# Kernel optimization log

Hardware: AMD Instinct MI355X
Metric: run time of the kernel (lower is better)

Reference implementation:

```python
import jax, jax.numpy as jnp
import numpy as np

N = 50000      # nodes of type 'conn'
E = 250000     # edges per edge type
NT = 3         # number of edge types
H = 3          # num_heads for hidden layers
D1, D2, DO = 64, 64, 32
IN0 = 34       # 8 + 3 + 6 + 17


def setup_inputs() -> dict:
    key = jax.random.key(0)
    ks = jax.random.split(key, 40)
    it = iter(range(40))

    def nrm(shape, scale=0.1):
        return jax.random.normal(ks[next(it)], shape, dtype=jnp.float32) * scale

    inp = {}
    inp["cat_inputs"] = jax.random.randint(ks[next(it)], (N, 3), 0, 5, dtype=jnp.int32)
    inp["cont_inputs"] = jax.random.normal(ks[next(it)], (N, 17), dtype=jnp.float32)
    inp["src"] = jax.random.randint(ks[next(it)], (NT, E), 0, N)
    inp["dst"] = jax.random.randint(ks[next(it)], (NT, E), 0, N)
    # embedding tables
    inp["emb0"] = nrm((14, 8))
    inp["emb1"] = nrm((5, 3))
    inp["emb2"] = nrm((10, 6))
    # layer 1: GATConv(34 -> 64, heads=3) per etype
    inp["W1"] = nrm((NT, IN0, H * D1))
    inp["al1"] = nrm((NT, H, D1))
    inp["ar1"] = nrm((NT, H, D1))
    inp["b1"] = nrm((NT, H * D1))
    # layer 2: GATConv(192 -> 64, heads=3) per etype
    inp["W2"] = nrm((NT, H * D1, H * D2))
    inp["al2"] = nrm((NT, H, D2))
    inp["ar2"] = nrm((NT, H, D2))
    inp["b2"] = nrm((NT, H * D2))
    # output layer: GATConv(192 -> 32, heads=1) per etype
    inp["W3"] = nrm((NT, H * D2, DO))
    inp["al3"] = nrm((NT, 1, DO))
    inp["ar3"] = nrm((NT, 1, DO))
    inp["b3"] = nrm((NT, DO))
    return inp


def _gat(x, W, al, ar, b, src_t, dst_t, heads, out):
    """DGL GATConv: linear -> per-edge LeakyReLU(0.2) attention -> edge softmax
    over incoming edges -> weighted scatter-sum -> +bias -> leaky_relu(0.01)."""
    n = x.shape[0]
    feat = (x @ W).reshape(n, heads, out)          # (N,H,D)
    el = jnp.sum(feat * al, axis=-1)               # (N,H)
    er = jnp.sum(feat * ar, axis=-1)               # (N,H)
    e = jax.nn.leaky_relu(el[src_t] + er[dst_t], 0.2)  # (E,H)
    emax = jax.ops.segment_max(e, dst_t, num_segments=n)   # (N,H), -inf for empty ok
    ee = jnp.exp(e - emax[dst_t])
    den = jax.ops.segment_sum(ee, dst_t, num_segments=n)
    alpha = ee / den[dst_t]                        # (E,H)
    msg = feat[src_t] * alpha[:, :, None]          # (E,H,D)
    rst = jax.ops.segment_sum(msg, dst_t, num_segments=n) + b.reshape(1, heads, out)
    return jax.nn.leaky_relu(rst, 0.01)            # GATConv activation=F.leaky_relu


def reference(cont_inputs, emb0, emb1, emb2,
              W1, al1, ar1, b1, W2, al2, ar2, b2, W3, al3, ar3, b3,
              cat_inputs, src, dst):
    x = jnp.concatenate([emb0[cat_inputs[:, 0]],
                         emb1[cat_inputs[:, 1]],
                         emb2[cat_inputs[:, 2]],
                         cont_inputs], axis=1)     # (N,34)

    def hetero(h, W, al, ar, b, heads, out):
        # HeteroGraphConv(aggregate='mean') over NT edge types, then flatten(1)
        outs = [_gat(h, W[t], al[t], ar[t], b[t], src[t], dst[t], heads, out)
                for t in range(NT)]
        agg = jnp.mean(jnp.stack(outs, 0), axis=0)  # (N,heads,out)
        return agg.reshape(h.shape[0], heads * out)

    h = hetero(x, W1, al1, ar1, b1, H, D1)
    h = hetero(h, W2, al2, ar2, b2, H, D2)
    h = hetero(h, W3, al3, ar3, b3, 1, DO)
    return h
```

## Files before the change

kernel.cpp:

```cpp
#include <hip/hip_runtime.h>

#define NNODES 50000
#define NEDGES 250000
#define NTYPES 3
#define SCAN_B ((NNODES + 255) / 256)
#define LSTR 40

typedef __attribute__((ext_vector_type(8))) short bf16x8;
typedef __attribute__((ext_vector_type(4))) float f32x4;

__device__ __forceinline__ float lrelu(float x, float s) { return x >= 0.f ? x : s * x; }

__device__ __forceinline__ unsigned short bf16_rne(float f) {
    unsigned u = __float_as_uint(f);
    unsigned r = (u + 0x7fffu + ((u >> 16) & 1u)) >> 16;
    return (unsigned short)r;
}
__device__ __forceinline__ float bf16_to_f(unsigned short h) {
    return __uint_as_float((unsigned)h << 16);
}

__global__ void build_x_kernel(const int* __restrict__ cat, const float* __restrict__ cont,
                               const float* __restrict__ e0, const float* __restrict__ e1,
                               const float* __restrict__ e2, short* __restrict__ Ahi,
                               short* __restrict__ Alo) {
    int n = blockIdx.x * 4 + (threadIdx.x >> 6);
    int k = threadIdx.x & 63;
    if (n >= NNODES) return;
    float v = 0.f;
    if (k < 8) v = e0[cat[n * 3 + 0] * 8 + k];
    else if (k < 11) v = e1[cat[n * 3 + 1] * 3 + (k - 8)];
    else if (k < 17) v = e2[cat[n * 3 + 2] * 6 + (k - 11)];
    else if (k < 34) v = cont[n * 17 + (k - 17)];
    unsigned short h = bf16_rne(v);
    float fh = bf16_to_f(h);
    unsigned short l = bf16_rne(v - fh);
    Ahi[(size_t)n * 64 + k] = (short)h;
    Alo[(size_t)n * 64 + k] = (short)l;
}

__global__ void hist_kernel(const int* __restrict__ dst, int* __restrict__ deg) {
    int idx = blockIdx.x * blockDim.x + threadIdx.x;
    if (idx >= NTYPES * NEDGES) return;
    int t = idx / NEDGES;
    atomicAdd(&deg[t * NNODES + dst[idx]], 1);
}

__global__ void scan1_kernel(const int* __restrict__ deg, int* __restrict__ rowptr,
                             int* __restrict__ bsum) {
    __shared__ int sd[256];
    int t = blockIdx.y, b = blockIdx.x, tid = threadIdx.x;
    int n = b * 256 + tid;
    int v = (n < NNODES) ? deg[t * NNODES + n] : 0;
    sd[tid] = v;
    __syncthreads();
    for (int off = 1; off < 256; off <<= 1) {
        int x = 0;
        if (tid >= off) x = sd[tid - off];
        __syncthreads();
        if (tid >= off) sd[tid] += x;
        __syncthreads();
    }
    int incl = sd[tid];
    if (n < NNODES) rowptr[(size_t)t * (NNODES + 1) + n] = incl - v;
    if (tid == 255) bsum[t * SCAN_B + b] = incl;
}

__global__ void scan2_kernel(int* __restrict__ bsum, int* __restrict__ rowptr) {
    int t = threadIdx.x;
    if (t >= NTYPES) return;
    int run = 0;
    for (int i = 0; i < SCAN_B; i++) {
        int v = bsum[t * SCAN_B + i];
        bsum[t * SCAN_B + i] = run;
        run += v;
    }
    rowptr[(size_t)t * (NNODES + 1) + NNODES] = run;
}

__global__ void scan3_kernel(const int* __restrict__ bsum, int* __restrict__ rowptr) {
    int t = blockIdx.y, b = blockIdx.x;
    int n = b * 256 + threadIdx.x;
    if (n < NNODES) rowptr[(size_t)t * (NNODES + 1) + n] += bsum[t * SCAN_B + b];
}

__global__ void scatter_kernel(const int* __restrict__ src, const int* __restrict__ dst,
                               const int* __restrict__ rowptr, int* __restrict__ cursor,
                               int* __restrict__ csrc) {
    int idx = blockIdx.x * blockDim.x + threadIdx.x;
    if (idx >= NTYPES * NEDGES) return;
    int t = idx / NEDGES;
    int s = src[idx], d = dst[idx];
    int pos = rowptr[(size_t)t * (NNODES + 1) + d] + atomicAdd(&cursor[t * NNODES + d], 1);
    csrc[(size_t)t * NEDGES + pos] = s;
}

__global__ void convert_B_kernel(const float* __restrict__ W, short* __restrict__ Bhi,
                                 short* __restrict__ Blo, int Kin, int Kout, int HD, int Mfeat) {
    int idx = blockIdx.x * blockDim.x + threadIdx.x;
    if (idx >= Mfeat * Kout) return;
    int m = idx / Kout, k = idx % Kout;
    int t = m / HD, j = m % HD;
    float a = (k < Kin) ? W[((size_t)t * Kin + k) * HD + j] : 0.f;
    unsigned short h = bf16_rne(a);
    float fh = bf16_to_f(h);
    unsigned short l = bf16_rne(a - fh);
    Bhi[(size_t)m * Kout + k] = (short)h;
    Blo[(size_t)m * Kout + k] = (short)l;
}

__global__ void convert_Bel_kernel(const float* __restrict__ W, const float* __restrict__ alw,
                                   const float* __restrict__ arw, short* __restrict__ Bhi,
                                   short* __restrict__ Blo, int Kin, int Kout, int H, int D,
                                   int Mfeat) {
    int idx = blockIdx.x * blockDim.x + threadIdx.x;
    if (idx >= 24 * Kout) return;
    int m = idx / Kout, k = idx % Kout;
    int t = m >> 3, r = m & 7;
    int h = r & 3;
    float v = 0.f;
    if (h < H && k < Kin) {
        const float* a = ((r >= 4) ? arw : alw) + ((size_t)t * H + h) * D;
        const float* w = W + ((size_t)t * Kin + k) * (H * D) + h * D;
        for (int j = 0; j < D; j++) v += w[j] * a[j];
    }
    unsigned short hh = bf16_rne(v);
    float fh = bf16_to_f(hh);
    unsigned short ll = bf16_rne(v - fh);
    size_t o = (size_t)(Mfeat + m) * Kout + k;
    Bhi[o] = (short)hh;
    Blo[o] = (short)ll;
}

__global__ __launch_bounds__(256) void gemm_mfma_kernel(
    const short* __restrict__ AhiG, const short* __restrict__ AloG,
    const short* __restrict__ BhiG, const short* __restrict__ BloG,
    unsigned short* __restrict__ feat, float* __restrict__ elr, int N, int K, int M, int Mfeat,
    int HD, size_t tstride, int MT) {
    __shared__ short smem[4 * 128 * LSTR];
    short* AsH = smem;
    short* AsL = smem + 128 * LSTR;
    short* BsH = smem + 2 * 128 * LSTR;
    short* BsL = smem + 3 * 128 * LSTR;
    int tid = threadIdx.x;

    int nwg = gridDim.x;
    int q = nwg >> 3, rr = nwg & 7;
    int xx = blockIdx.x & 7, ii = blockIdx.x >> 3;
    int wg = (xx < rr ? xx * (q + 1) : rr * (q + 1) + (xx - rr) * q) + ii;
    int m0 = (wg % MT) * 128, n0 = (wg / MT) * 128;

    int wid = tid >> 6, lane = tid & 63;
    int wm = (wid >> 1) * 64, wn = (wid & 1) * 64;
    int lrow = lane & 15, kq = (lane >> 4) * 8;
    int sr = tid >> 2;
    int skq = (tid & 3) * 8;
    f32x4 acc[4][4] = {};

    for (int k0 = 0; k0 < K; k0 += 32) {
        __syncthreads();
#pragma unroll
        for (int p = 0; p < 2; p++) {
            const bf16x8 z = {};
            bf16x8 vh = z, vl = z;
            int gr = n0 + sr + p * 64;
            if (gr < N) {
                size_t o = (size_t)gr * K + k0 + skq;
                vh = *(const bf16x8*)(AhiG + o);
                vl = *(const bf16x8*)(AloG + o);
            }
            *(bf16x8*)&AsH[(sr + p * 64) * LSTR + skq] = vh;
            *(bf16x8*)&AsL[(sr + p * 64) * LSTR + skq] = vl;
            vh = z;
            vl = z;
            int gc = m0 + sr + p * 64;
            if (gc < M) {
                size_t o = (size_t)gc * K + k0 + skq;
                vh = *(const bf16x8*)(BhiG + o);
                vl = *(const bf16x8*)(BloG + o);
            }
            *(bf16x8*)&BsH[(sr + p * 64) * LSTR + skq] = vh;
            *(bf16x8*)&BsL[(sr + p * 64) * LSTR + skq] = vl;
        }
        __syncthreads();
        bf16x8 ah[4], al[4], bh[4], bl[4];
#pragma unroll
        for (int f = 0; f < 4; f++) {
            int ra = (wm + f * 16 + lrow) * LSTR + kq;
            ah[f] = *(const bf16x8*)&AsH[ra];
            al[f] = *(const bf16x8*)&AsL[ra];
            int rb = (wn + f * 16 + lrow) * LSTR + kq;
            bh[f] = *(const bf16x8*)&BsH[rb];
            bl[f] = *(const bf16x8*)&BsL[rb];
        }
#pragma unroll
        for (int fa = 0; fa < 4; fa++)
#pragma unroll
            for (int fb = 0; fb < 4; fb++) {
                acc[fa][fb] =
                    __builtin_amdgcn_mfma_f32_16x16x32_bf16(al[fa], bh[fb], acc[fa][fb], 0, 0, 0);
                acc[fa][fb] =
                    __builtin_amdgcn_mfma_f32_16x16x32_bf16(ah[fa], bl[fb], acc[fa][fb], 0, 0, 0);
                acc[fa][fb] =
                    __builtin_amdgcn_mfma_f32_16x16x32_bf16(ah[fa], bh[fb], acc[fa][fb], 0, 0, 0);
            }
    }

    __syncthreads();
    short* Ct = smem;
#pragma unroll
    for (int fb = 0; fb < 4; fb++) {
        int col = wn + fb * 16 + lrow;
        int gc = m0 + col;
#pragma unroll
        for (int fa = 0; fa < 4; fa++) {
            int rbase = wm + fa * 16 + (lane >> 4) * 4;
#pragma unroll
            for (int e = 0; e < 4; e++) {
                Ct[(rbase + e) * 136 + col] = (short)bf16_rne(acc[fa][fb][e]);
                if (gc >= Mfeat && gc < M) {
                    int gr = n0 + rbase + e;
                    if (gr < N) {
                        int m = gc - Mfeat;
                        int t = m >> 3, r = m & 7;
                        elr[((size_t)t * N + gr) * 8 + r] = acc[fa][fb][e];
                    }
                }
            }
        }
    }
    __syncthreads();
    int row = tid >> 1, half = tid & 1;
    int gr = n0 + row;
    if (gr < N) {
#pragma unroll
        for (int p = 0; p < 4; p++) {
            int col0 = half * 64 + p * 16;
            int gc0 = m0 + col0;
            if (gc0 < Mfeat) {
                int t = gc0 / HD, j = gc0 - t * HD;
                bf16x8 v0 = *(const bf16x8*)&Ct[row * 136 + col0];
                bf16x8 v1 = *(const bf16x8*)&Ct[row * 136 + col0 + 8];
                unsigned short* dp = feat + (size_t)t * tstride + (size_t)gr * HD + j;
                *(bf16x8*)dp = v0;
                *(bf16x8*)(dp + 8) = v1;
            }
        }
    }
}

template <int H>
__global__ void alpha_kernel(const int* __restrict__ rowptr_all, const int* __restrict__ csrc_all,
                             const float* __restrict__ elr, float* __restrict__ alpha_all) {
    int idx = blockIdx.x * blockDim.x + threadIdx.x;
    if (idx >= NTYPES * NNODES) return;
    int t = idx / NNODES, node = idx - t * NNODES;
    const int* rowptr = rowptr_all + t * (NNODES + 1);
    const int* csrc = csrc_all + (size_t)t * NEDGES;
    const float* elr_t = elr + (size_t)t * NNODES * 8;
    float4* alpha4 = (float4*)(alpha_all + (size_t)t * NEDGES * 4);
    float4 er4 = *(const float4*)(elr_t + (size_t)node * 8 + 4);
    float erd[3] = {er4.x, er4.y, er4.z};
    int rs = rowptr[node], re = rowptr[node + 1];
    float den[H];
#pragma unroll
    for (int h = 0; h < H; h++) den[h] = 0.f;
    for (int k = rs; k < re; k++) {
        int s = csrc[k];
        float4 e4 = *(const float4*)(elr_t + (size_t)s * 8);
        float ev[3] = {e4.x, e4.y, e4.z};
        float w[4] = {0.f, 0.f, 0.f, 0.f};
#pragma unroll
        for (int h = 0; h < H; h++) {
            w[h] = __expf(lrelu(ev[h] + erd[h], 0.2f));
            den[h] += w[h];
        }
        alpha4[k] = (float4){w[0], w[1], w[2], w[3]};
    }
    float inv[H];
#pragma unroll
    for (int h = 0; h < H; h++) inv[h] = __frcp_rn(den[h]);
    for (int k = rs; k < re; k++) {
        float4 w = alpha4[k];
        w.x *= inv[0];
        if (H > 1) {
            w.y *= inv[1];
            w.z *= inv[2];
        }
        alpha4[k] = w;
    }
}

template <int H, int D, int BF16OUT>
__global__ __launch_bounds__(256) void gat_agg_kernel(
    const int* __restrict__ rowptr_all, const int* __restrict__ csrc_all,
    const float* __restrict__ alpha_all, const unsigned short* __restrict__ feat_all,
    const float* __restrict__ b_all, float* __restrict__ fout, short* __restrict__ Ahi,
    short* __restrict__ Alo) {
    constexpr int HD = H * D;
    constexpr int EL = (HD + 63) / 64;
    int lane = threadIdx.x & 63;
    int node = blockIdx.x * 4 + (threadIdx.x >> 6);
    if (node >= NNODES) return;
    float out[EL] = {};
#pragma unroll 1
    for (int t = 0; t < NTYPES; t++) {
        const int* rowptr = rowptr_all + t * (NNODES + 1);
        const int* csrc = csrc_all + (size_t)t * NEDGES;
        const float4* alpha4 = (const float4*)(alpha_all + (size_t)t * NEDGES * 4);
        const unsigned short* feat = feat_all + (size_t)t * NNODES * HD;
        int rs = rowptr[node], re = rowptr[node + 1];
        float acc[EL] = {};
        for (int k = rs; k < re; k += 4) {
            int cnt = re - k;
            int s[4];
            float4 w4[4];
#pragma unroll
            for (int c = 0; c < 4; c++) {
                s[c] = csrc[k + (c < cnt ? c : 0)];
                w4[c] = (c < cnt) ? alpha4[k + c] : (float4){0.f, 0.f, 0.f, 0.f};
            }
#pragma unroll
            for (int c = 0; c < 4; c++) {
                float wv[3] = {w4[c].x, w4[c].y, w4[c].z};
#pragma unroll
                for (int q = 0; q < EL; q++) {
                    int j = lane + q * 64;
                    constexpr bool full = (HD % 64 == 0);
                    float fv = 0.f;
                    if (full || lane < (HD % 64) || q < EL - 1)
                        fv = bf16_to_f(feat[(size_t)s[c] * HD + j]);
                    int hh = (D == 64) ? q : 0;
                    acc[q] = fmaf(wv[hh], fv, acc[q]);
                }
            }
        }
#pragma unroll
        for (int q = 0; q < EL; q++) {
            int j = lane + q * 64;
            if (HD % 64 == 0 || j < HD) {
                float v = lrelu(acc[q] + b_all[t * HD + j], 0.01f);
                out[q] += v * (1.f / 3.f);
            }
        }
    }
#pragma unroll
    for (int q = 0; q < EL; q++) {
        int j = lane + q * 64;
        if (HD % 64 == 0 || j < HD) {
            if (BF16OUT) {
                unsigned short h = bf16_rne(out[q]);
                float fh = bf16_to_f(h);
                unsigned short l = bf16_rne(out[q] - fh);
                Ahi[(size_t)node * HD + j] = (short)h;
                Alo[(size_t)node * HD + j] = (short)l;
            } else {
                fout[(size_t)node * HD + j] = out[q];
            }
        }
    }
}

extern "C" void kernel_launch(void* const* d_in, const int* in_sizes, int n_in, void* d_out,
                              int out_size, void* d_ws, size_t ws_size, hipStream_t stream) {
    const int* cat = (const int*)d_in[0];
    const float* cont = (const float*)d_in[1];
    const int* src = (const int*)d_in[2];
    const int* dst = (const int*)d_in[3];
    const float* emb0 = (const float*)d_in[4];
    const float* emb1 = (const float*)d_in[5];
    const float* emb2 = (const float*)d_in[6];
    const float* W1 = (const float*)d_in[7];
    const float* al1 = (const float*)d_in[8];
    const float* ar1 = (const float*)d_in[9];
    const float* b1 = (const float*)d_in[10];
    const float* W2 = (const float*)d_in[11];
    const float* al2 = (const float*)d_in[12];
    const float* ar2 = (const float*)d_in[13];
    const float* b2 = (const float*)d_in[14];
    const float* W3 = (const float*)d_in[15];
    const float* al3 = (const float*)d_in[16];
    const float* ar3 = (const float*)d_in[17];
    const float* b3 = (const float*)d_in[18];

    unsigned short* feat_all = (unsigned short*)d_ws;
    short* Ahi = (short*)(feat_all + (size_t)3 * NNODES * 192);
    short* Alo = Ahi + (size_t)NNODES * 192;
    short* Bhi = Alo + (size_t)NNODES * 192;
    short* Blo = Bhi + 600 * 192;
    float* elr = (float*)(Blo + 600 * 192);
    float* alpha_all = elr + (size_t)3 * NNODES * 8;
    int* rowptr = (int*)(alpha_all + (size_t)3 * NEDGES * 4);
    int* csrc = rowptr + NTYPES * (NNODES + 1);
    int* deg = csrc + NTYPES * NEDGES;
    int* cursor = deg + NTYPES * NNODES;
    int* bsum = cursor + NTYPES * NNODES;

    hipMemsetAsync(deg, 0, (size_t)NTYPES * NNODES * 4, stream);
    hipMemsetAsync(cursor, 0, (size_t)NTYPES * NNODES * 4, stream);
    hist_kernel<<<(NTYPES * NEDGES + 255) / 256, 256, 0, stream>>>(dst, deg);
    scan1_kernel<<<dim3(SCAN_B, NTYPES), 256, 0, stream>>>(deg, rowptr, bsum);
    scan2_kernel<<<1, 64, 0, stream>>>(bsum, rowptr);
    scan3_kernel<<<dim3(SCAN_B, NTYPES), 256, 0, stream>>>(bsum, rowptr);
    scatter_kernel<<<(NTYPES * NEDGES + 255) / 256, 256, 0, stream>>>(src, dst, rowptr, cursor,
                                                                      csrc);

    build_x_kernel<<<(NNODES + 3) / 4, 256, 0, stream>>>(cat, cont, emb0, emb1, emb2, Ahi, Alo);

    const int gy = (NNODES + 127) / 128;
    const int aggb = (NNODES + 3) / 4;
    const int nb = (NTYPES * NNODES + 255) / 256;

    convert_B_kernel<<<(576 * 64 + 255) / 256, 256, 0, stream>>>(W1, Bhi, Blo, 34, 64, 192, 576);
    convert_Bel_kernel<<<(24 * 64 + 255) / 256, 256, 0, stream>>>(W1, al1, ar1, Bhi, Blo, 34, 64, 3,
                                                                  64, 576);
    gemm_mfma_kernel<<<5 * gy, 256, 0, stream>>>(Ahi, Alo, Bhi, Blo, feat_all, elr, NNODES, 64, 600,
                                                 576, 192, (size_t)NNODES * 192, 5);
    alpha_kernel<3><<<nb, 256, 0, stream>>>(rowptr, csrc, elr, alpha_all);
    gat_agg_kernel<3, 64, 1><<<aggb, 256, 0, stream>>>(rowptr, csrc, alpha_all, feat_all, b1,
                                                       nullptr, Ahi, Alo);

    convert_B_kernel<<<(576 * 192 + 255) / 256, 256, 0, stream>>>(W2, Bhi, Blo, 192, 192, 192, 576);
    convert_Bel_kernel<<<(24 * 192 + 255) / 256, 256, 0, stream>>>(W2, al2, ar2, Bhi, Blo, 192, 192,
                                                                   3, 64, 576);
    gemm_mfma_kernel<<<5 * gy, 256, 0, stream>>>(Ahi, Alo, Bhi, Blo, feat_all, elr, NNODES, 192,
                                                 600, 576, 192, (size_t)NNODES * 192, 5);
    alpha_kernel<3><<<nb, 256, 0, stream>>>(rowptr, csrc, elr, alpha_all);
    gat_agg_kernel<3, 64, 1><<<aggb, 256, 0, stream>>>(rowptr, csrc, alpha_all, feat_all, b2,
                                                       nullptr, Ahi, Alo);

    convert_B_kernel<<<(96 * 192 + 255) / 256, 256, 0, stream>>>(W3, Bhi, Blo, 192, 192, 32, 96);
    convert_Bel_kernel<<<(24 * 192 + 255) / 256, 256, 0, stream>>>(W3, al3, ar3, Bhi, Blo, 192, 192,
                                                                   1, 32, 96);
    gemm_mfma_kernel<<<1 * gy, 256, 0, stream>>>(Ahi, Alo, Bhi, Blo, feat_all, elr, NNODES, 192,
                                                 120, 96, 32, (size_t)NNODES * 32, 1);
    alpha_kernel<1><<<nb, 256, 0, stream>>>(rowptr, csrc, elr, alpha_all);
    gat_agg_kernel<1, 32, 0><<<aggb, 256, 0, stream>>>(rowptr, csrc, alpha_all, feat_all, b3,
                                                       (float*)d_out, nullptr, nullptr);
}
```

Measured before the change: 533.2 us.

## Merge per-type CSR into node-major combined CSR and defer softmax normalization

Builds a combined node-major CSR in which each destination node's edges for all three edge types sit contiguously, with a per-node int4 of type boundaries. Source indices are stored pre-offset by type. The aggregation kernel then walks a single edge range per node, using a ballot-controlled loop and per-type accumulators. The alpha kernel drops its second normalization pass and stores reciprocal denominators that are applied after aggregation. The 32-wide output layer packs two nodes per wavefront and stores scalar alphas, in exchange for branchy per-edge type selection and an extra small kernel.

```diff
diff --git a/kernel.cpp b/kernel.cpp
--- a/kernel.cpp
+++ b/kernel.cpp
@@ -84,15 +84,28 @@
     if (n < NNODES) rowptr[(size_t)t * (NNODES + 1) + n] += bsum[t * SCAN_B + b];
 }
 
+__global__ void cbase_kernel(const int* __restrict__ rowptr, int4* __restrict__ cbase4) {
+    int n = blockIdx.x * blockDim.x + threadIdx.x;
+    if (n >= NNODES) return;
+    int r0 = rowptr[n], r0e = rowptr[n + 1];
+    int r1 = rowptr[(NNODES + 1) + n], r1e = rowptr[(NNODES + 1) + n + 1];
+    int r2 = rowptr[2 * (NNODES + 1) + n], r2e = rowptr[2 * (NNODES + 1) + n + 1];
+    int b0 = r0 + r1 + r2;
+    int b1 = b0 + (r0e - r0);
+    int b2 = b1 + (r1e - r1);
+    int b3 = b2 + (r2e - r2);
+    cbase4[n] = (int4){b0, b1, b2, b3};
+}
+
 __global__ void scatter_kernel(const int* __restrict__ src, const int* __restrict__ dst,
-                               const int* __restrict__ rowptr, int* __restrict__ cursor,
-                               int* __restrict__ csrc) {
+                               const int* __restrict__ cbase, int* __restrict__ cursor,
+                               int* __restrict__ csrc_c) {
     int idx = blockIdx.x * blockDim.x + threadIdx.x;
     if (idx >= NTYPES * NEDGES) return;
     int t = idx / NEDGES;
     int s = src[idx], d = dst[idx];
-    int pos = rowptr[(size_t)t * (NNODES + 1) + d] + atomicAdd(&cursor[t * NNODES + d], 1);
-    csrc[(size_t)t * NEDGES + pos] = s;
+    int pos = cbase[(size_t)d * 4 + t] + atomicAdd(&cursor[t * NNODES + d], 1);
+    csrc_c[pos] = t * NNODES + s;
 }
 
 __global__ void convert_B_kernel(const float* __restrict__ W, short* __restrict__ Bhi,
@@ -250,113 +263,128 @@
 }
 
 template <int H>
-__global__ void alpha_kernel(const int* __restrict__ rowptr_all, const int* __restrict__ csrc_all,
-                             const float* __restrict__ elr, float* __restrict__ alpha_all) {
+__global__ void alpha_kernel(const int4* __restrict__ cbase4, const int* __restrict__ csrc_c,
+                             const float* __restrict__ elr, float* __restrict__ alpha_c,
+                             float4* __restrict__ invden4) {
     int idx = blockIdx.x * blockDim.x + threadIdx.x;
     if (idx >= NTYPES * NNODES) return;
     int t = idx / NNODES, node = idx - t * NNODES;
-    const int* rowptr = rowptr_all + t * (NNODES + 1);
-    const int* csrc = csrc_all + (size_t)t * NEDGES;
-    const float* elr_t = elr + (size_t)t * NNODES * 8;
-    float4* alpha4 = (float4*)(alpha_all + (size_t)t * NEDGES * 4);
-    float4 er4 = *(const float4*)(elr_t + (size_t)node * 8 + 4);
+    int4 cb = cbase4[node];
+    int rs = (t == 0) ? cb.x : (t == 1) ? cb.y : cb.z;
+    int re = (t == 0) ? cb.y : (t == 1) ? cb.z : cb.w;
+    float4 er4 = *(const float4*)(elr + ((size_t)t * NNODES + node) * 8 + 4);
     float erd[3] = {er4.x, er4.y, er4.z};
-    int rs = rowptr[node], re = rowptr[node + 1];
     float den[H];
 #pragma unroll
     for (int h = 0; h < H; h++) den[h] = 0.f;
     for (int k = rs; k < re; k++) {
-        int s = csrc[k];
-        float4 e4 = *(const float4*)(elr_t + (size_t)s * 8);
+        int cs = csrc_c[k];
+        float4 e4 = *(const float4*)(elr + (size_t)cs * 8);
         float ev[3] = {e4.x, e4.y, e4.z};
-        float w[4] = {0.f, 0.f, 0.f, 0.f};
+        float w[3] = {0.f, 0.f, 0.f};
 #pragma unroll
         for (int h = 0; h < H; h++) {
             w[h] = __expf(lrelu(ev[h] + erd[h], 0.2f));
             den[h] += w[h];
         }
-        alpha4[k] = (float4){w[0], w[1], w[2], w[3]};
-    }
-    float inv[H];
-#pragma unroll
-    for (int h = 0; h < H; h++) inv[h] = __frcp_rn(den[h]);
-    for (int k = rs; k < re; k++) {
-        float4 w = alpha4[k];
-        w.x *= inv[0];
+        if (H == 1)
+            alpha_c[k] = w[0];
+        else
+            *(float4*)(alpha_c + (size_t)k * 4) = (float4){w[0], w[1], w[2], 0.f};
+    }
+    float4 iv = {0.f, 0.f, 0.f, 0.f};
+    if (re > rs) {
+        iv.x = __frcp_rn(den[0]);
         if (H > 1) {
-            w.y *= inv[1];
-            w.z *= inv[2];
-        }
-        alpha4[k] = w;
-    }
+            iv.y = __frcp_rn(den[1]);
+            iv.z = __frcp_rn(den[2]);
+        }
+    }
+    invden4[idx] = iv;
 }
 
 template <int H, int D, int BF16OUT>
 __global__ __launch_bounds__(256) void gat_agg_kernel(
-    const int* __restrict__ rowptr_all, const int* __restrict__ csrc_all,
-    const float* __restrict__ alpha_all, const unsigned short* __restrict__ feat_all,
-    const float* __restrict__ b_all, float* __restrict__ fout, short* __restrict__ Ahi,
-    short* __restrict__ Alo) {
+    const int4* __restrict__ cbase4, const int* __restrict__ csrc_c,
+    const float* __restrict__ alpha_c, const float4* __restrict__ invden4,
+    const unsigned short* __restrict__ feat_all, const float* __restrict__ b_all,
+    float* __restrict__ fout, short* __restrict__ Ahi, short* __restrict__ Alo) {
     constexpr int HD = H * D;
-    constexpr int EL = (HD + 63) / 64;
+    constexpr int LPN = (D == 64) ? 64 : 32;
+    constexpr int NPW = 64 / LPN;
+    constexpr int EL = HD / LPN;
     int lane = threadIdx.x & 63;
-    int node = blockIdx.x * 4 + (threadIdx.x >> 6);
+    int j0 = lane & (LPN - 1);
+    int node = blockIdx.x * (4 * NPW) + (threadIdx.x >> 6) * NPW + ((NPW == 2) ? (lane >> 5) : 0);
     if (node >= NNODES) return;
+    int4 cb = cbase4[node];
+    int ks = cb.x, ke = cb.w;
+    float acc[3][EL] = {};
+    for (int it = 0;; ++it) {
+        int k = ks + it * 4;
+        if (!__ballot(k < ke)) break;
+        int cnt = ke - k;
+        int cs[4];
+        float4 w4[4];
+#pragma unroll
+        for (int c = 0; c < 4; c++) {
+            int kk = (c < cnt) ? (k + c) : min(ks, NTYPES * NEDGES - 1);
+            cs[c] = csrc_c[kk];
+            if (H == 1) {
+                float wv = (c < cnt) ? alpha_c[kk] : 0.f;
+                w4[c] = (float4){wv, 0.f, 0.f, 0.f};
+            } else {
+                w4[c] = (c < cnt) ? *(const float4*)(alpha_c + (size_t)kk * 4)
+                                  : (float4){0.f, 0.f, 0.f, 0.f};
+            }
+        }
+#pragma unroll
+        for (int c = 0; c < 4; c++) {
+            int t = (cs[c] >= NNODES) + (cs[c] >= 2 * NNODES);
+            float wq[3] = {w4[c].x, w4[c].y, w4[c].z};
+            float fv[EL];
+#pragma unroll
+            for (int q = 0; q < EL; q++)
+                fv[q] = bf16_to_f(feat_all[(size_t)cs[c] * HD + j0 + q * LPN]);
+            if (t == 0) {
+#pragma unroll
+                for (int q = 0; q < EL; q++)
+                    acc[0][q] = fmaf((D == 64) ? wq[q] : wq[0], fv[q], acc[0][q]);
+            } else if (t == 1) {
+#pragma unroll
+                for (int q = 0; q < EL; q++)
+                    acc[1][q] = fmaf((D == 64) ? wq[q] : wq[0], fv[q], acc[1][q]);
+            } else {
+#pragma unroll
+                for (int q = 0; q < EL; q++)
+                    acc[2][q] = fmaf((D == 64) ? wq[q] : wq[0], fv[q], acc[2][q]);
+            }
+        }
+    }
     float out[EL] = {};
-#pragma unroll 1
-    for (int t = 0; t < NTYPES; t++) {
-        const int* rowptr = rowptr_all + t * (NNODES + 1);
-        const int* csrc = csrc_all + (size_t)t * NEDGES;
-        const float4* alpha4 = (const float4*)(alpha_all + (size_t)t * NEDGES * 4);
-        const unsigned short* feat = feat_all + (size_t)t * NNODES * HD;
-        int rs = rowptr[node], re = rowptr[node + 1];
-        float acc[EL] = {};
-        for (int k = rs; k < re; k += 4) {
-            int cnt = re - k;
-            int s[4];
-            float4 w4[4];
-#pragma unroll
-            for (int c = 0; c < 4; c++) {
-                s[c] = csrc[k + (c < cnt ? c : 0)];
-                w4[c] = (c < cnt) ? alpha4[k + c] : (float4){0.f, 0.f, 0.f, 0.f};
-            }
-#pragma unroll
-            for (int c = 0; c < 4; c++) {
-                float wv[3] = {w4[c].x, w4[c].y, w4[c].z};
-#pragma unroll
-                for (int q = 0; q < EL; q++) {
-                    int j = lane + q * 64;
-                    constexpr bool full = (HD % 64 == 0);
-                    float fv = 0.f;
-                    if (full || lane < (HD % 64) || q < EL - 1)
-                        fv = bf16_to_f(feat[(size_t)s[c] * HD + j]);
-                    int hh = (D == 64) ? q : 0;
-                    acc[q] = fmaf(wv[hh], fv, acc[q]);
-                }
-            }
-        }
+#pragma unroll
+    for (int t = 0; t < 3; t++) {
+        float4 iv = invden4[(size_t)t * NNODES + node];
+        float ivq[3] = {iv.x, iv.y, iv.z};
 #pragma unroll
         for (int q = 0; q < EL; q++) {
-            int j = lane + q * 64;
-            if (HD % 64 == 0 || j < HD) {
-                float v = lrelu(acc[q] + b_all[t * HD + j], 0.01f);
-                out[q] += v * (1.f / 3.f);
-            }
+            int j = j0 + q * LPN;
+            float v = acc[t][q] * ((D == 64) ? ivq[q] : ivq[0]);
+            v = lrelu(v + b_all[t * HD + j], 0.01f);
+            out[q] += v * (1.f / 3.f);
         }
     }
 #pragma unroll
     for (int q = 0; q < EL; q++) {
-        int j = lane + q * 64;
-        if (HD % 64 == 0 || j < HD) {
-            if (BF16OUT) {
-                unsigned short h = bf16_rne(out[q]);
-                float fh = bf16_to_f(h);
-                unsigned short l = bf16_rne(out[q] - fh);
-                Ahi[(size_t)node * HD + j] = (short)h;
-                Alo[(size_t)node * HD + j] = (short)l;
-            } else {
-                fout[(size_t)node * HD + j] = out[q];
-            }
+        int j = j0 + q * LPN;
+        if (BF16OUT) {
+            unsigned short h = bf16_rne(out[q]);
+            float fh = bf16_to_f(h);
+            unsigned short l = bf16_rne(out[q] - fh);
+            Ahi[(size_t)node * HD + j] = (short)h;
+            Alo[(size_t)node * HD + j] = (short)l;
+        } else {
+            fout[(size_t)node * HD + j] = out[q];
         }
     }
 }
@@ -389,10 +417,12 @@
     short* Bhi = Alo + (size_t)NNODES * 192;
     short* Blo = Bhi + 600 * 192;
     float* elr = (float*)(Blo + 600 * 192);
-    float* alpha_all = elr + (size_t)3 * NNODES * 8;
-    int* rowptr = (int*)(alpha_all + (size_t)3 * NEDGES * 4);
-    int* csrc = rowptr + NTYPES * (NNODES + 1);
-    int* deg = csrc + NTYPES * NEDGES;
+    float* alpha_c = elr + (size_t)3 * NNODES * 8;
+    float4* invden4 = (float4*)(alpha_c + (size_t)3 * NEDGES * 4);
+    int4* cbase4 = (int4*)(invden4 + (size_t)3 * NNODES);
+    int* rowptr = (int*)(cbase4 + NNODES);
+    int* csrc_c = rowptr + NTYPES * (NNODES + 1);
+    int* deg = csrc_c + NTYPES * NEDGES;
     int* cursor = deg + NTYPES * NNODES;
     int* bsum = cursor + NTYPES * NNODES;
 
@@ -402,39 +432,41 @@
     scan1_kernel<<<dim3(SCAN_B, NTYPES), 256, 0, stream>>>(deg, rowptr, bsum);
     scan2_kernel<<<1, 64, 0, stream>>>(bsum, rowptr);
     scan3_kernel<<<dim3(SCAN_B, NTYPES), 256, 0, stream>>>(bsum, rowptr);
-    scatter_kernel<<<(NTYPES * NEDGES + 255) / 256, 256, 0, stream>>>(src, dst, rowptr, cursor,
-                                                                      csrc);
+    cbase_kernel<<<(NNODES + 255) / 256, 256, 0, stream>>>(rowptr, cbase4);
+    scatter_kernel<<<(NTYPES * NEDGES + 255) / 256, 256, 0, stream>>>(src, dst, (const int*)cbase4,
+                                                                      cursor, csrc_c);
 
     build_x_kernel<<<(NNODES + 3) / 4, 256, 0, stream>>>(cat, cont, emb0, emb1, emb2, Ahi, Alo);
 
     const int gy = (NNODES + 127) / 128;
-    const int aggb = (NNODES + 3) / 4;
     const int nb = (NTYPES * NNODES + 255) / 256;
+    const int aggb64 = (NNODES + 3) / 4;
+    const int aggb32 = (NNODES + 7) / 8;
 
     convert_B_kernel<<<(576 * 64 + 255) / 256, 256, 0, stream>>>(W1, Bhi, Blo, 34, 64, 192, 576);
     convert_Bel_kernel<<<(24 * 64 + 255) / 256, 256, 0, stream>>>(W1, al1, ar1, Bhi, Blo, 34, 64, 3,
                                                                   64, 576);
     gemm_mfma_kernel<<<5 * gy, 256, 0, stream>>>(Ahi, Alo, Bhi, Blo, feat_all, elr, NNODES, 64, 600,
                                                  576, 192, (size_t)NNODES * 192, 5);
-    alpha_kernel<3><<<nb, 256, 0, stream>>>(rowptr, csrc, elr, alpha_all);
-    gat_agg_kernel<3, 64, 1><<<aggb, 256, 0, stream>>>(rowptr, csrc, alpha_all, feat_all, b1,
-                                                       nullptr, Ahi, Alo);
+    alpha_kernel<3><<<nb, 256, 0, stream>>>(cbase4, csrc_c, elr, alpha_c, invden4);
+    gat_agg_kernel<3, 64, 1><<<aggb64, 256, 0, stream>>>(cbase4, csrc_c, alpha_c, invden4, feat_all,
+                                                         b1, nullptr, Ahi, Alo);
 
     convert_B_kernel<<<(576 * 192 + 255) / 256, 256, 0, stream>>>(W2, Bhi, Blo, 192, 192, 192, 576);
     convert_Bel_kernel<<<(24 * 192 + 255) / 256, 256, 0, stream>>>(W2, al2, ar2, Bhi, Blo, 192, 192,
                                                                    3, 64, 576);
     gemm_mfma_kernel<<<5 * gy, 256, 0, stream>>>(Ahi, Alo, Bhi, Blo, feat_all, elr, NNODES, 192,
                                                  600, 576, 192, (size_t)NNODES * 192, 5);
-    alpha_kernel<3><<<nb, 256, 0, stream>>>(rowptr, csrc, elr, alpha_all);
-    gat_agg_kernel<3, 64, 1><<<aggb, 256, 0, stream>>>(rowptr, csrc, alpha_all, feat_all, b2,
-                                                       nullptr, Ahi, Alo);
+    alpha_kernel<3><<<nb, 256, 0, stream>>>(cbase4, csrc_c, elr, alpha_c, invden4);
+    gat_agg_kernel<3, 64, 1><<<aggb64, 256, 0, stream>>>(cbase4, csrc_c, alpha_c, invden4, feat_all,
+                                                         b2, nullptr, Ahi, Alo);
 
     convert_B_kernel<<<(96 * 192 + 255) / 256, 256, 0, stream>>>(W3, Bhi, Blo, 192, 192, 32, 96);
     convert_Bel_kernel<<<(24 * 192 + 255) / 256, 256, 0, stream>>>(W3, al3, ar3, Bhi, Blo, 192, 192,
                                                                    1, 32, 96);
     gemm_mfma_kernel<<<1 * gy, 256, 0, stream>>>(Ahi, Alo, Bhi, Blo, feat_all, elr, NNODES, 192,
                                                  120, 96, 32, (size_t)NNODES * 32, 1);
-    alpha_kernel<1><<<nb, 256, 0, stream>>>(rowptr, csrc, elr, alpha_all);
-    gat_agg_kernel<1, 32, 0><<<aggb, 256, 0, stream>>>(rowptr, csrc, alpha_all, feat_all, b3,
-                                                       (float*)d_out, nullptr, nullptr);
-}
+    alpha_kernel<1><<<nb, 256, 0, stream>>>(cbase4, csrc_c, elr, alpha_c, invden4);
+    gat_agg_kernel<1, 32, 0><<<aggb32, 256, 0, stream>>>(cbase4, csrc_c, alpha_c, invden4, feat_all,
+                                                         b3, (float*)d_out, nullptr, nullptr);
+}
```

Result: slower. 559.4 us (+4.9%).

## Defer softmax normalization to aggregation and pack two nodes per wave for final layer

Applied to the files above, without the earlier changes.

The alpha kernel no longer makes a second pass over each node's edges to normalize weights. It stores unnormalized exp weights plus a per-node reciprocal denominator, and the aggregation kernel multiplies by that reciprocal after summing. The H=1 layer stores a scalar alpha per edge instead of a float4. The final 32-wide layer maps two nodes per 64-lane wave so no lanes sit idle. This removes a read-modify-write over the alpha array and halves the wasted lanes in the last aggregation, at the cost of one extra small per-node load.

```diff
diff --git a/kernel.cpp b/kernel.cpp
--- a/kernel.cpp
+++ b/kernel.cpp
@@ -251,14 +251,14 @@
 
 template <int H>
 __global__ void alpha_kernel(const int* __restrict__ rowptr_all, const int* __restrict__ csrc_all,
-                             const float* __restrict__ elr, float* __restrict__ alpha_all) {
+                             const float* __restrict__ elr, float* __restrict__ alpha_all,
+                             float4* __restrict__ invden4) {
     int idx = blockIdx.x * blockDim.x + threadIdx.x;
     if (idx >= NTYPES * NNODES) return;
     int t = idx / NNODES, node = idx - t * NNODES;
     const int* rowptr = rowptr_all + t * (NNODES + 1);
     const int* csrc = csrc_all + (size_t)t * NEDGES;
     const float* elr_t = elr + (size_t)t * NNODES * 8;
-    float4* alpha4 = (float4*)(alpha_all + (size_t)t * NEDGES * 4);
     float4 er4 = *(const float4*)(elr_t + (size_t)node * 8 + 4);
     float erd[3] = {er4.x, er4.y, er4.z};
     int rs = rowptr[node], re = rowptr[node + 1];
@@ -269,45 +269,47 @@
         int s = csrc[k];
         float4 e4 = *(const float4*)(elr_t + (size_t)s * 8);
         float ev[3] = {e4.x, e4.y, e4.z};
-        float w[4] = {0.f, 0.f, 0.f, 0.f};
+        float w[3] = {0.f, 0.f, 0.f};
 #pragma unroll
         for (int h = 0; h < H; h++) {
             w[h] = __expf(lrelu(ev[h] + erd[h], 0.2f));
             den[h] += w[h];
         }
-        alpha4[k] = (float4){w[0], w[1], w[2], w[3]};
-    }
-    float inv[H];
-#pragma unroll
-    for (int h = 0; h < H; h++) inv[h] = __frcp_rn(den[h]);
-    for (int k = rs; k < re; k++) {
-        float4 w = alpha4[k];
-        w.x *= inv[0];
+        if (H == 1)
+            alpha_all[(size_t)t * NEDGES + k] = w[0];
+        else
+            *(float4*)(alpha_all + ((size_t)t * NEDGES + k) * 4) = (float4){w[0], w[1], w[2], 0.f};
+    }
+    float4 iv = {0.f, 0.f, 0.f, 0.f};
+    if (re > rs) {
+        iv.x = __frcp_rn(den[0]);
         if (H > 1) {
-            w.y *= inv[1];
-            w.z *= inv[2];
-        }
-        alpha4[k] = w;
-    }
+            iv.y = __frcp_rn(den[1]);
+            iv.z = __frcp_rn(den[2]);
+        }
+    }
+    invden4[idx] = iv;
 }
 
 template <int H, int D, int BF16OUT>
 __global__ __launch_bounds__(256) void gat_agg_kernel(
     const int* __restrict__ rowptr_all, const int* __restrict__ csrc_all,
-    const float* __restrict__ alpha_all, const unsigned short* __restrict__ feat_all,
-    const float* __restrict__ b_all, float* __restrict__ fout, short* __restrict__ Ahi,
-    short* __restrict__ Alo) {
+    const float* __restrict__ alpha_all, const float4* __restrict__ invden4,
+    const unsigned short* __restrict__ feat_all, const float* __restrict__ b_all,
+    float* __restrict__ fout, short* __restrict__ Ahi, short* __restrict__ Alo) {
     constexpr int HD = H * D;
-    constexpr int EL = (HD + 63) / 64;
+    constexpr int LPN = (D == 64) ? 64 : 32;
+    constexpr int NPW = 64 / LPN;
+    constexpr int EL = HD / LPN;
     int lane = threadIdx.x & 63;
-    int node = blockIdx.x * 4 + (threadIdx.x >> 6);
+    int j0 = lane & (LPN - 1);
+    int node = blockIdx.x * (4 * NPW) + (threadIdx.x >> 6) * NPW + ((NPW == 2) ? (lane >> 5) : 0);
     if (node >= NNODES) return;
     float out[EL] = {};
 #pragma unroll 1
     for (int t = 0; t < NTYPES; t++) {
         const int* rowptr = rowptr_all + t * (NNODES + 1);
         const int* csrc = csrc_all + (size_t)t * NEDGES;
-        const float4* alpha4 = (const float4*)(alpha_all + (size_t)t * NEDGES * 4);
         const unsigned short* feat = feat_all + (size_t)t * NNODES * HD;
         int rs = rowptr[node], re = rowptr[node + 1];
         float acc[EL] = {};
@@ -317,46 +319,47 @@
             float4 w4[4];
 #pragma unroll
             for (int c = 0; c < 4; c++) {
-                s[c] = csrc[k + (c < cnt ? c : 0)];
-                w4[c] = (c < cnt) ? alpha4[k + c] : (float4){0.f, 0.f, 0.f, 0.f};
+                int kk = k + (c < cnt ? c : 0);
+                s[c] = csrc[kk];
+                if (H == 1) {
+                    float wv = alpha_all[(size_t)t * NEDGES + kk];
+                    w4[c] = (float4){(c < cnt) ? wv : 0.f, 0.f, 0.f, 0.f};
+                } else {
+                    w4[c] = (c < cnt) ? *(const float4*)(alpha_all + ((size_t)t * NEDGES + kk) * 4)
+                                      : (float4){0.f, 0.f, 0.f, 0.f};
+                }
             }
 #pragma unroll
             for (int c = 0; c < 4; c++) {
-                float wv[3] = {w4[c].x, w4[c].y, w4[c].z};
+                float wq[3] = {w4[c].x, w4[c].y, w4[c].z};
 #pragma unroll
                 for (int q = 0; q < EL; q++) {
-                    int j = lane + q * 64;
-                    constexpr bool full = (HD % 64 == 0);
-                    float fv = 0.f;
-                    if (full || lane < (HD % 64) || q < EL - 1)
-                        fv = bf16_to_f(feat[(size_t)s[c] * HD + j]);
-                    int hh = (D == 64) ? q : 0;
-                    acc[q] = fmaf(wv[hh], fv, acc[q]);
+                    float fv = bf16_to_f(feat[(size_t)s[c] * HD + j0 + q * LPN]);
+                    acc[q] = fmaf((D == 64) ? wq[q] : wq[0], fv, acc[q]);
                 }
             }
         }
+        float4 iv = invden4[(size_t)t * NNODES + node];
+        float ivq[3] = {iv.x, iv.y, iv.z};
 #pragma unroll
         for (int q = 0; q < EL; q++) {
-            int j = lane + q * 64;
-            if (HD % 64 == 0 || j < HD) {
-                float v = lrelu(acc[q] + b_all[t * HD + j], 0.01f);
-                out[q] += v * (1.f / 3.f);
-            }
+            int j = j0 + q * LPN;
+            float v = acc[q] * ((D == 64) ? ivq[q] : ivq[0]);
+            v = lrelu(v + b_all[t * HD + j], 0.01f);
+            out[q] += v * (1.f / 3.f);
         }
     }
 #pragma unroll
     for (int q = 0; q < EL; q++) {
-        int j = lane + q * 64;
-        if (HD % 64 == 0 || j < HD) {
-            if (BF16OUT) {
-                unsigned short h = bf16_rne(out[q]);
-                float fh = bf16_to_f(h);
-                unsigned short l = bf16_rne(out[q] - fh);
-                Ahi[(size_t)node * HD + j] = (short)h;
-                Alo[(size_t)node * HD + j] = (short)l;
-            } else {
-                fout[(size_t)node * HD + j] = out[q];
-            }
+        int j = j0 + q * LPN;
+        if (BF16OUT) {
+            unsigned short h = bf16_rne(out[q]);
+            float fh = bf16_to_f(h);
+            unsigned short l = bf16_rne(out[q] - fh);
+            Ahi[(size_t)node * HD + j] = (short)h;
+            Alo[(size_t)node * HD + j] = (short)l;
+        } else {
+            fout[(size_t)node * HD + j] = out[q];
         }
     }
 }
@@ -390,7 +393,8 @@
     short* Blo = Bhi + 600 * 192;
     float* elr = (float*)(Blo + 600 * 192);
     float* alpha_all = elr + (size_t)3 * NNODES * 8;
-    int* rowptr = (int*)(alpha_all + (size_t)3 * NEDGES * 4);
+    float4* invden4 = (float4*)(alpha_all + (size_t)3 * NEDGES * 4);
+    int* rowptr = (int*)(invden4 + (size_t)3 * NNODES);
     int* csrc = rowptr + NTYPES * (NNODES + 1);
     int* deg = csrc + NTYPES * NEDGES;
     int* cursor = deg + NTYPES * NNODES;
@@ -408,33 +412,34 @@
     build_x_kernel<<<(NNODES + 3) / 4, 256, 0, stream>>>(cat, cont, emb0, emb1, emb2, Ahi, Alo);
 
     const int gy = (NNODES + 127) / 128;
-    const int aggb = (NNODES + 3) / 4;
     const int nb = (NTYPES * NNODES + 255) / 256;
+    const int aggb64 = (NNODES + 3) / 4;
+    const int aggb32 = (NNODES + 7) / 8;
 
     convert_B_kernel<<<(576 * 64 + 255) / 256, 256, 0, stream>>>(W1, Bhi, Blo, 34, 64, 192, 576);
     convert_Bel_kernel<<<(24 * 64 + 255) / 256, 256, 0, stream>>>(W1, al1, ar1, Bhi, Blo, 34, 64, 3,
                                                                   64, 576);
     gemm_mfma_kernel<<<5 * gy, 256, 0, stream>>>(Ahi, Alo, Bhi, Blo, feat_all, elr, NNODES, 64, 600,
                                                  576, 192, (size_t)NNODES * 192, 5);
-    alpha_kernel<3><<<nb, 256, 0, stream>>>(rowptr, csrc, elr, alpha_all);
-    gat_agg_kernel<3, 64, 1><<<aggb, 256, 0, stream>>>(rowptr, csrc, alpha_all, feat_all, b1,
-                                                       nullptr, Ahi, Alo);
+    alpha_kernel<3><<<nb, 256, 0, stream>>>(rowptr, csrc, elr, alpha_all, invden4);
+    gat_agg_kernel<3, 64, 1><<<aggb64, 256, 0, stream>>>(rowptr, csrc, alpha_all, invden4, feat_all,
+                                                         b1, nullptr, Ahi, Alo);
 
     convert_B_kernel<<<(576 * 192 + 255) / 256, 256, 0, stream>>>(W2, Bhi, Blo, 192, 192, 192, 576);
     convert_Bel_kernel<<<(24 * 192 + 255) / 256, 256, 0, stream>>>(W2, al2, ar2, Bhi, Blo, 192, 192,
                                                                    3, 64, 576);
     gemm_mfma_kernel<<<5 * gy, 256, 0, stream>>>(Ahi, Alo, Bhi, Blo, feat_all, elr, NNODES, 192,
                                                  600, 576, 192, (size_t)NNODES * 192, 5);
-    alpha_kernel<3><<<nb, 256, 0, stream>>>(rowptr, csrc, elr, alpha_all);
-    gat_agg_kernel<3, 64, 1><<<aggb, 256, 0, stream>>>(rowptr, csrc, alpha_all, feat_all, b2,
-                                                       nullptr, Ahi, Alo);
+    alpha_kernel<3><<<nb, 256, 0, stream>>>(rowptr, csrc, elr, alpha_all, invden4);
+    gat_agg_kernel<3, 64, 1><<<aggb64, 256, 0, stream>>>(rowptr, csrc, alpha_all, invden4, feat_all,
+                                                         b2, nullptr, Ahi, Alo);
 
     convert_B_kernel<<<(96 * 192 + 255) / 256, 256, 0, stream>>>(W3, Bhi, Blo, 192, 192, 32, 96);
     convert_Bel_kernel<<<(24 * 192 + 255) / 256, 256, 0, stream>>>(W3, al3, ar3, Bhi, Blo, 192, 192,
                                                                    1, 32, 96);
     gemm_mfma_kernel<<<1 * gy, 256, 0, stream>>>(Ahi, Alo, Bhi, Blo, feat_all, elr, NNODES, 192,
                                                  120, 96, 32, (size_t)NNODES * 32, 1);
-    alpha_kernel<1><<<nb, 256, 0, stream>>>(rowptr, csrc, elr, alpha_all);
-    gat_agg_kernel<1, 32, 0><<<aggb, 256, 0, stream>>>(rowptr, csrc, alpha_all, feat_all, b3,
-                                                       (float*)d_out, nullptr, nullptr);
-}
+    alpha_kernel<1><<<nb, 256, 0, stream>>>(rowptr, csrc, elr, alpha_all, invden4);
+    gat_agg_kernel<1, 32, 0><<<aggb32, 256, 0, stream>>>(rowptr, csrc, alpha_all, invden4, feat_all,
+                                                         b3, (float*)d_out, nullptr, nullptr);
+}
```

After: 472.7 us. 1.13x faster.
